# Optimization experiments

Measured on AMD Instinct MI355X. Metric: run time of the kernel, lower is better.

## Reference

```python
import jax, jax.numpy as jnp
import numpy as np
from jax import lax

TAU = 2.0      # LIF membrane time constant
VTH = 0.5      # spike threshold
ALPHA = 4.0    # sigmoid surrogate gradient sharpness (spikingjelly default)
EPS = 1e-5     # BatchNorm eps
HEADS = 8

@jax.custom_vjp
def _spike(x):
    return (x >= 0.0).astype(x.dtype)

def _spike_fwd(x):
    return _spike(x), x

def _spike_bwd(x, g):
    s = jax.nn.sigmoid(ALPHA * x)
    return (g * ALPHA * s * (1.0 - s),)

_spike.defvjp(_spike_fwd, _spike_bwd)

def lif(x_seq):
    # multi-step LIF, decay_input=True, hard reset to 0, detach_reset=True
    def step(v, x):
        v = v + (x - v) / TAU
        s = _spike(v - VTH)
        v = v * (1.0 - lax.stop_gradient(s))
        return v, s
    _, s_seq = lax.scan(step, jnp.zeros_like(x_seq[0]), x_seq)
    return s_seq

def bn(x, gamma, beta, mean, var):
    # inference-mode BatchNorm over channel axis 2 of [T,B,C,H,W]
    sh = (1, 1, -1, 1, 1)
    scale = gamma.reshape(sh) / jnp.sqrt(var.reshape(sh) + EPS)
    return (x - mean.reshape(sh)) * scale + beta.reshape(sh)

def conv1x1(x, w, b=None):
    y = jnp.einsum('oc,tbchw->tbohw', w, x)
    if b is not None:
        y = y + b.reshape(1, 1, -1, 1, 1)
    return y

def setup_inputs() -> dict:
    key = jax.random.key(0)
    T, B, C, H, W = 4, 8, 384, 32, 32
    ks = jax.random.split(key, 20)
    s = 1.0 / np.sqrt(C)
    d = {
        'x': jax.random.normal(ks[0], (T, B, C, H, W), jnp.float32),
        'q_w': jax.random.normal(ks[1], (C, C), jnp.float32) * s,
        'k_w': jax.random.normal(ks[2], (C, C), jnp.float32) * s,
        'v_w': jax.random.normal(ks[3], (C, C), jnp.float32) * s,
        'th_w': jax.random.normal(ks[4], (HEADS, HEADS), jnp.float32) * (1.0 / np.sqrt(HEADS)),
        'proj_w': jax.random.normal(ks[5], (C, C), jnp.float32) * s,
        'proj_b': jax.random.normal(ks[6], (C,), jnp.float32) * 0.01,
    }
    for i, p in enumerate(['q', 'k', 'v', 'proj']):
        kk = jax.random.split(ks[7 + i], 4)
        d[f'{p}_gamma'] = 1.0 + 0.1 * jax.random.normal(kk[0], (C,), jnp.float32)
        d[f'{p}_beta'] = 0.1 * jax.random.normal(kk[1], (C,), jnp.float32)
        d[f'{p}_mean'] = 0.1 * jax.random.normal(kk[2], (C,), jnp.float32)
        d[f'{p}_var'] = jax.random.uniform(kk[3], (C,), jnp.float32, 0.5, 1.5)
    return d

def reference(x, q_w, k_w, v_w, th_w, proj_w, proj_b,
              q_gamma, q_beta, q_mean, q_var,
              k_gamma, k_beta, k_mean, k_var,
              v_gamma, v_beta, v_mean, v_var,
              proj_gamma, proj_beta, proj_mean, proj_var):
    T, B, C, H, W = x.shape
    hd = C // HEADS
    N = H * W
    identity = x
    xs = lif(x)  # shortcut_lif

    def branch(w, g, be, m, va):
        return lif(bn(conv1x1(xs, w), g, be, m, va))

    def split_heads(t):  # [T,B,C,H,W] -> [T,B,heads,N,hd]
        return t.reshape(T, B, HEADS, hd, N).transpose(0, 1, 2, 4, 3)

    q = split_heads(branch(q_w, q_gamma, q_beta, q_mean, q_var))
    k = split_heads(branch(k_w, k_gamma, k_beta, k_mean, k_var))
    v = split_heads(branch(v_w, v_gamma, v_beta, v_mean, v_var))

    kv = (k * v).sum(axis=3)                      # [T,B,heads,hd]
    kv = jnp.einsum('oh,tbhd->tbod', th_w, kv)     # talking heads (Conv1d 1x1, no bias)
    kv = lif(kv)[:, :, :, None, :]                 # [T,B,heads,1,hd]

    x_att = q * kv                                 # broadcast over N
    x_att = x_att.transpose(0, 1, 2, 4, 3).reshape(T, B, C, H, W)
    out = bn(conv1x1(x_att, proj_w, proj_b), proj_gamma, proj_beta, proj_mean, proj_var)
    return out + identity
```

## Files before the change

### kernel.cpp

```cpp
#include <hip/hip_runtime.h>
#include <stdint.h>


typedef unsigned short u16;
typedef __attribute__((ext_vector_type(8))) short short8v;
typedef __attribute__((ext_vector_type(4))) float f32x4;

#define AS1 __attribute__((address_space(1)))
#define AS3 __attribute__((address_space(3)))

__device__ __forceinline__ void async16(const void* g, void* l) {
    __builtin_amdgcn_global_load_lds((const AS1 unsigned int*)g,
                                     (AS3 unsigned int*)l, 16, 0, 0);
}
__device__ __forceinline__ f32x4 mfma_bf16(short8v a, short8v b, f32x4 c) {
    return __builtin_amdgcn_mfma_f32_16x16x32_bf16(a, b, c, 0, 0, 0);
}
__device__ __forceinline__ f32x4 mfma_f16(short8v a, short8v b, f32x4 c) {
    return __builtin_amdgcn_mfma_f32_16x16x32_f16(a, b, c, 0, 0, 0);
}

__device__ __forceinline__ u16 f2bf(float f) {
    uint32_t x = __float_as_uint(f);
    return (u16)((x + 0x7FFFu + ((x >> 16) & 1u)) >> 16);
}

#define SPIKE_H ((u16)0x3C00)
#define SPIKE_B ((u16)0x3F80)

__global__ void prep_kernel(const float* __restrict__ qw, const float* __restrict__ kw,
                            const float* __restrict__ vw, const float* __restrict__ pw,
                            u16* __restrict__ Ah, u16* __restrict__ Aproj) {
    int id = blockIdx.x * 256 + threadIdx.x;
    if (id >= 1152 * 384) return;
    int m = id / 384, c = id % 384;
    int br = m / 384, o = m % 384;
    const float* W = (br == 0) ? qw : (br == 1) ? kw : vw;
    float w = W[o * 384 + c];
    union H { _Float16 h; u16 u; } u0, u1;
    u0.h = (_Float16)w;
    float r1 = w - (float)u0.h;
    u1.h = (_Float16)r1;
    u16* row = Ah + (size_t)m * 768;
    row[c] = u0.u;
    row[384 + c] = u1.u;
    if (br == 0) Aproj[o * 384 + c] = f2bf(pw[o * 384 + c]);
}

__global__ __launch_bounds__(256) void lifx_kernel(const float* __restrict__ x,
                                                   u16* __restrict__ xs) {
    __shared__ u16 Tr[64 * 72];
    int b = blockIdx.z, c0 = blockIdx.y * 64, n0 = blockIdx.x * 64;
    int tid = threadIdx.x;
    int nj = (tid & 15) * 4;
    int ci = tid >> 4;
    float v[4][4];
#pragma unroll
    for (int p = 0; p < 4; p++)
#pragma unroll
        for (int e = 0; e < 4; e++) v[p][e] = 0.0f;

    for (int t = 0; t < 4; t++) {
#pragma unroll
        for (int p = 0; p < 4; p++) {
            const float* src = x + ((size_t)((t * 8 + b) * 384 + c0 + p * 16 + ci)) * 1024 + n0 + nj;
            float4 xv = *(const float4*)src;
            float xa[4] = {xv.x, xv.y, xv.z, xv.w};
#pragma unroll
            for (int e = 0; e < 4; e++) {
                float vv = v[p][e];
                vv = __fadd_rn(vv, __fmul_rn(__fsub_rn(xa[e], vv), 0.5f));
                bool sp = (vv >= 0.5f);
                v[p][e] = sp ? 0.0f : vv;
                Tr[(nj + e) * 72 + p * 16 + ci] = sp ? SPIKE_H : (u16)0;
            }
        }
        __syncthreads();
#pragma unroll
        for (int p = 0; p < 4; p++) {
            int nr = p * 16 + (tid >> 4);
            int c4 = (tid & 15) * 4;
            *(ushort4*)(xs + ((size_t)((t * 8 + b) * 1024 + n0 + nr)) * 384 + c0 + c4) =
                *(const ushort4*)&Tr[nr * 72 + c4];
        }
        __syncthreads();
    }
}

__global__ __launch_bounds__(256, 2) void qkv_kernel(
    const u16* __restrict__ Ah, const u16* __restrict__ xs,
    u16* __restrict__ qs, u16* __restrict__ ks, u16* __restrict__ vs,
    const float* __restrict__ qg, const float* __restrict__ qb, const float* __restrict__ qm, const float* __restrict__ qv,
    const float* __restrict__ kg, const float* __restrict__ kb, const float* __restrict__ km, const float* __restrict__ kvr,
    const float* __restrict__ vg, const float* __restrict__ vb, const float* __restrict__ vm, const float* __restrict__ vvr) {
    __shared__ __align__(16) u16 At[2][8192];
    __shared__ __align__(16) u16 Bt[2][8192];
    __shared__ __align__(16) float bnS[128];
    __shared__ __align__(16) float bnM[128];
    __shared__ __align__(16) float bnB[128];

    int b = blockIdx.z, mt = blockIdx.y, nt = blockIdx.x;
    int m0 = mt * 128, n0 = nt * 128;
    int branch = mt / 3, o0 = (mt % 3) * 128;
    int tid = threadIdx.x, wave = tid >> 6, lane = tid & 63;
    int l15 = lane & 15, quad = lane >> 4;
    int wm = (wave & 1) * 64, wn = (wave >> 1) * 64;

    const float* g_ = (branch == 0) ? qg : (branch == 1) ? kg : vg;
    const float* be_ = (branch == 0) ? qb : (branch == 1) ? kb : vb;
    const float* m_ = (branch == 0) ? qm : (branch == 1) ? km : vm;
    const float* v_ = (branch == 0) ? qv : (branch == 1) ? kvr : vvr;
    u16* dstp = (branch == 0) ? qs : (branch == 1) ? ks : vs;

    if (tid < 128) {
        int o = o0 + tid;
        bnS[tid] = g_[o] / sqrtf(v_[o] + 1e-5f);
        bnM[tid] = m_[o];
        bnB[tid] = be_[o];
    }

    auto stage = [&](int s) {
        int st = s / 12, kkb = s % 12;
        int buf = s & 1;
        int kk = kkb * 64;
        int ck = (kk >= 384) ? kk - 384 : kk;
        const u16* Bsrc = xs + ((size_t)((st * 8 + b) * 1024 + n0)) * 384;
#pragma unroll
        for (int ii = 0; ii < 4; ii++) {
            int l = ii * 256 + tid;
            int row = l >> 3;
            int cs = (l & 7) ^ (row & 7);
            async16(Ah + (size_t)(m0 + row) * 768 + kk + cs * 8, &At[buf][l * 8]);
            async16(Bsrc + (size_t)row * 384 + ck + cs * 8, &Bt[buf][l * 8]);
        }
    };

    float vmem[4][4][4];
#pragma unroll
    for (int i = 0; i < 4; i++)
#pragma unroll
        for (int j = 0; j < 4; j++)
#pragma unroll
            for (int e = 0; e < 4; e++) vmem[i][j][e] = 0.0f;

    stage(0);
    __syncthreads();

    for (int t = 0; t < 4; t++) {
        f32x4 acc[4][4];
#pragma unroll
        for (int i = 0; i < 4; i++)
#pragma unroll
            for (int j = 0; j < 4; j++) acc[i][j] = (f32x4){0.f, 0.f, 0.f, 0.f};

        for (int kkb = 0; kkb < 12; kkb++) {
            int s = t * 12 + kkb;
            int buf = s & 1;
            if (s + 1 < 48) stage(s + 1);
#pragma unroll
            for (int h = 0; h < 2; h++) {
                short8v af[4], bfr[4];
#pragma unroll
                for (int i = 0; i < 4; i++) {
                    int row = wm + i * 16 + l15;
                    int ch = (h * 4 + quad) ^ (row & 7);
                    af[i] = *(const short8v*)&At[buf][row * 64 + ch * 8];
                }
#pragma unroll
                for (int j = 0; j < 4; j++) {
                    int nr = wn + j * 16 + l15;
                    int ch = (h * 4 + quad) ^ (nr & 7);
                    bfr[j] = *(const short8v*)&Bt[buf][nr * 64 + ch * 8];
                }
#pragma unroll
                for (int i = 0; i < 4; i++)
#pragma unroll
                    for (int j = 0; j < 4; j++) acc[i][j] = mfma_f16(af[i], bfr[j], acc[i][j]);
            }
            __syncthreads();
        }

        size_t rb = (size_t)((t * 8 + b) * 1024 + n0);
#pragma unroll
        for (int i = 0; i < 4; i++) {
            int co = wm + i * 16 + quad * 4;
            float4 sc4 = *(const float4*)&bnS[co];
            float4 mn4 = *(const float4*)&bnM[co];
            float4 bt4 = *(const float4*)&bnB[co];
            float scA[4] = {sc4.x, sc4.y, sc4.z, sc4.w};
            float mnA[4] = {mn4.x, mn4.y, mn4.z, mn4.w};
            float btA[4] = {bt4.x, bt4.y, bt4.z, bt4.w};
#pragma unroll
            for (int j = 0; j < 4; j++) {
                int n = wn + j * 16 + l15;
                u16 sv[4];
#pragma unroll
                for (int e = 0; e < 4; e++) {
                    float a = acc[i][j][e];
                    a = __fadd_rn(__fmul_rn(__fsub_rn(a, mnA[e]), scA[e]), btA[e]);
                    float vv = vmem[i][j][e];
                    vv = __fadd_rn(vv, __fmul_rn(__fsub_rn(a, vv), 0.5f));
                    bool sp = (vv >= 0.5f);
                    vmem[i][j][e] = sp ? 0.0f : vv;
                    sv[e] = sp ? SPIKE_B : (u16)0;
                }
                ushort4 s4;
                s4.x = sv[0]; s4.y = sv[1]; s4.z = sv[2]; s4.w = sv[3];
                *(ushort4*)(dstp + (rb + n) * 384 + o0 + co) = s4;
            }
        }
    }
}

__global__ void kvred_kernel(const u16* __restrict__ ks, const u16* __restrict__ vs,
                             float* __restrict__ r) {
    __shared__ float red[384];
    int tb = blockIdx.y, nc = blockIdx.x;
    int tid = threadIdx.x;
    int rr = tid / 48, c8 = tid % 48;
    red[tid] = 0.0f;
    __syncthreads();

    float cnt[8];
#pragma unroll
    for (int e = 0; e < 8; e++) cnt[e] = 0.0f;

    size_t base = ((size_t)(tb * 1024 + nc * 64 + rr)) * 384 + c8 * 8;
#pragma unroll 2
    for (int it = 0; it < 8; it++) {
        size_t off = base + (size_t)it * 8 * 384;
        uint4 ka = *(const uint4*)(ks + off);
        uint4 va = *(const uint4*)(vs + off);
        uint32_t w0 = ka.x & va.x, w1 = ka.y & va.y, w2 = ka.z & va.z, w3 = ka.w & va.w;
        const uint32_t S = SPIKE_B;
        if ((w0 & 0xFFFFu) == S) cnt[0] += 1.0f;
        if ((w0 >> 16) == S)     cnt[1] += 1.0f;
        if ((w1 & 0xFFFFu) == S) cnt[2] += 1.0f;
        if ((w1 >> 16) == S)     cnt[3] += 1.0f;
        if ((w2 & 0xFFFFu) == S) cnt[4] += 1.0f;
        if ((w2 >> 16) == S)     cnt[5] += 1.0f;
        if ((w3 & 0xFFFFu) == S) cnt[6] += 1.0f;
        if ((w3 >> 16) == S)     cnt[7] += 1.0f;
    }
#pragma unroll
    for (int e = 0; e < 8; e++) atomicAdd(&red[c8 * 8 + e], cnt[e]);
    __syncthreads();
    atomicAdd(&r[tb * 384 + tid], red[tid]);
}

__global__ void talking_kernel(const float* __restrict__ r, const float* __restrict__ th,
                               u16* __restrict__ kvs) {
    int id = blockIdx.x * 256 + threadIdx.x;
    if (id >= 8 * 384) return;
    int b = id / 384, c = id % 384;
    int oh = c / 48, d = c % 48;
    float v = 0.0f;
    for (int t = 0; t < 4; t++) {
        const float* rr = r + (t * 8 + b) * 384 + d;
        float s = 0.0f;
#pragma unroll
        for (int h = 0; h < 8; h++) s = __fmaf_rn(th[oh * 8 + h], rr[h * 48], s);
        v = __fadd_rn(v, __fmul_rn(__fsub_rn(s, v), 0.5f));
        bool sp = (v >= 0.5f);
        v = sp ? 0.0f : v;
        kvs[(t * 8 + b) * 384 + c] = sp ? SPIKE_B : (u16)0;
    }
}

__global__ __launch_bounds__(256, 2) void proj_kernel(
    const u16* __restrict__ Aproj, const u16* __restrict__ qs, const u16* __restrict__ kvs,
    const float* __restrict__ xin,
    const float* __restrict__ pb, const float* __restrict__ pg, const float* __restrict__ pbe,
    const float* __restrict__ pm, const float* __restrict__ pv, float* __restrict__ out) {
    __shared__ __align__(16) u16 At[2][8192];
    __shared__ __align__(16) u16 Bt[2][8192];

    int tb = blockIdx.z, mt = blockIdx.y, nt = blockIdx.x;
    int m0 = mt * 128, n0 = nt * 128;
    int tid = threadIdx.x, wave = tid >> 6, lane = tid & 63;
    int l15 = lane & 15, quad = lane >> 4;
    int wm = (wave & 1) * 64, wn = (wave >> 1) * 64;

    const u16* Bsrc = qs + ((size_t)(tb * 1024 + n0)) * 384;
    const u16* mbase = kvs + tb * 384;

    auto stage = [&](int s) {
        int kk = s * 64;
        int buf = s & 1;
#pragma unroll
        for (int ii = 0; ii < 4; ii++) {
            int l = ii * 256 + tid;
            int row = l >> 3;
            int cs = (l & 7) ^ (row & 7);
            async16(Aproj + (size_t)(m0 + row) * 384 + kk + cs * 8, &At[buf][l * 8]);
            async16(Bsrc + (size_t)row * 384 + kk + cs * 8, &Bt[buf][l * 8]);
        }
    };

    f32x4 acc[4][4];
#pragma unroll
    for (int i = 0; i < 4; i++)
#pragma unroll
        for (int j = 0; j < 4; j++) acc[i][j] = (f32x4){0.f, 0.f, 0.f, 0.f};

    stage(0);
    __syncthreads();

    for (int kkb = 0; kkb < 6; kkb++) {
        int buf = kkb & 1;
        int kk = kkb * 64;
        if (kkb + 1 < 6) stage(kkb + 1);
#pragma unroll
        for (int h = 0; h < 2; h++) {
            int g = h * 4 + quad;
            short8v msk = *(const short8v*)(mbase + kk + g * 8);
            short8v af[4], bfr[4];
#pragma unroll
            for (int i = 0; i < 4; i++) {
                int row = wm + i * 16 + l15;
                int ch = g ^ (row & 7);
                af[i] = *(const short8v*)&At[buf][row * 64 + ch * 8];
            }
#pragma unroll
            for (int j = 0; j < 4; j++) {
                int nr = wn + j * 16 + l15;
                int ch = g ^ (nr & 7);
                bfr[j] = *(const short8v*)&Bt[buf][nr * 64 + ch * 8] & msk;
            }
#pragma unroll
            for (int i = 0; i < 4; i++)
#pragma unroll
                for (int j = 0; j < 4; j++) acc[i][j] = mfma_bf16(af[i], bfr[j], acc[i][j]);
        }
        __syncthreads();
    }

#pragma unroll
    for (int i = 0; i < 4; i++) {
#pragma unroll
        for (int e = 0; e < 4; e++) {
            int o = m0 + wm + i * 16 + quad * 4 + e;
            float scale = pg[o] / sqrtf(pv[o] + 1e-5f);
            float mean = pm[o], beta = pbe[o], bias = pb[o];
#pragma unroll
            for (int j = 0; j < 4; j++) {
                int n = n0 + wn + j * 16 + l15;
                size_t idx = ((size_t)tb * 384 + o) * 1024 + n;
                float y = __fadd_rn(acc[i][j][e], bias);
                y = __fadd_rn(__fmul_rn(__fsub_rn(y, mean), scale), beta);
                out[idx] = __fadd_rn(y, xin[idx]);
            }
        }
    }
}

extern "C" void kernel_launch(void* const* d_in, const int* in_sizes, int n_in,
                              void* d_out, int out_size, void* d_ws, size_t ws_size,
                              hipStream_t stream) {
    (void)in_sizes; (void)n_in; (void)out_size; (void)ws_size;
    const float* x  = (const float*)d_in[0];
    const float* qw = (const float*)d_in[1];
    const float* kw = (const float*)d_in[2];
    const float* vw = (const float*)d_in[3];
    const float* th = (const float*)d_in[4];
    const float* pw = (const float*)d_in[5];
    const float* pb = (const float*)d_in[6];
    const float* qg = (const float*)d_in[7],  *qbe = (const float*)d_in[8];
    const float* qm = (const float*)d_in[9],  *qv  = (const float*)d_in[10];
    const float* kg = (const float*)d_in[11], *kbe = (const float*)d_in[12];
    const float* km = (const float*)d_in[13], *kv_ = (const float*)d_in[14];
    const float* vg = (const float*)d_in[15], *vbe = (const float*)d_in[16];
    const float* vm = (const float*)d_in[17], *vv_ = (const float*)d_in[18];
    const float* pg = (const float*)d_in[19], *pbe = (const float*)d_in[20];
    const float* pm = (const float*)d_in[21], *pv  = (const float*)d_in[22];
    float* out = (float*)d_out;

    char* w = (char*)d_ws;
    const size_t SPIKES = (size_t)32 * 1024 * 384 * 2;
    u16* xs    = (u16*)(w);
    u16* qs    = (u16*)(w + SPIKES);
    u16* ks    = (u16*)(w + 2 * SPIKES);
    u16* vs    = (u16*)(w + 3 * SPIKES);
    u16* Ah    = (u16*)(w + 4 * SPIKES);
    u16* Aproj = (u16*)(w + 4 * SPIKES + 1769472);
    float* r   = (float*)(w + 4 * SPIKES + 1769472 + 294912);
    u16* kvs   = (u16*)(w + 4 * SPIKES + 1769472 + 294912 + 49152);

    hipMemsetAsync(r, 0, 32 * 384 * sizeof(float), stream);

    prep_kernel<<<1728, 256, 0, stream>>>(qw, kw, vw, pw, Ah, Aproj);
    lifx_kernel<<<dim3(16, 6, 8), 256, 0, stream>>>(x, xs);
    qkv_kernel<<<dim3(8, 9, 8), 256, 0, stream>>>(Ah, xs, qs, ks, vs,
                                                  qg, qbe, qm, qv,
                                                  kg, kbe, km, kv_,
                                                  vg, vbe, vm, vv_);
    kvred_kernel<<<dim3(16, 32), 384, 0, stream>>>(ks, vs, r);
    talking_kernel<<<12, 256, 0, stream>>>(r, th, kvs);
    proj_kernel<<<dim3(8, 3, 32), 256, 0, stream>>>(Aproj, qs, kvs, x, pb, pg, pbe, pm, pv, out);
}
```

Baseline: 299.1 us.

## Restructure QKV GEMM to batch all timesteps into one 512-thread tile

The QKV kernel now uses 512 threads and loads B tiles for all four timesteps at once, so each A fragment is reused across four timesteps. A single 24-step K loop replaces the per-timestep loop, and the LIF recurrence runs over timesteps in registers in the epilogue. The loop uses a two-stage async prefetch with explicit vmcnt/lgkmcnt waits and barriers, plus s_setprio around the MFMA block. BN parameters are read directly from global memory instead of shared memory. The cost is a larger accumulator set (4x8 tiles per wave), which raises register pressure at launch bounds of 512 threads and 4 blocks.

Result: slower. 943.1 us (+215.4%).

```diff
diff --git a/kernel.cpp b/kernel.cpp
--- a/kernel.cpp
+++ b/kernel.cpp
@@ -87,126 +87,129 @@
     }
 }
 
-__global__ __launch_bounds__(256, 2) void qkv_kernel(
+__global__ __launch_bounds__(512, 4) void qkv_kernel(
     const u16* __restrict__ Ah, const u16* __restrict__ xs,
     u16* __restrict__ qs, u16* __restrict__ ks, u16* __restrict__ vs,
     const float* __restrict__ qg, const float* __restrict__ qb, const float* __restrict__ qm, const float* __restrict__ qv,
     const float* __restrict__ kg, const float* __restrict__ kb, const float* __restrict__ km, const float* __restrict__ kvr,
     const float* __restrict__ vg, const float* __restrict__ vb, const float* __restrict__ vm, const float* __restrict__ vvr) {
-    __shared__ __align__(16) u16 At[2][8192];
-    __shared__ __align__(16) u16 Bt[2][8192];
-    __shared__ __align__(16) float bnS[128];
-    __shared__ __align__(16) float bnM[128];
-    __shared__ __align__(16) float bnB[128];
+    __shared__ __align__(16) u16 At[2][4096];
+    __shared__ __align__(16) u16 Bt[2][16384];
 
     int b = blockIdx.z, mt = blockIdx.y, nt = blockIdx.x;
     int m0 = mt * 128, n0 = nt * 128;
     int branch = mt / 3, o0 = (mt % 3) * 128;
     int tid = threadIdx.x, wave = tid >> 6, lane = tid & 63;
     int l15 = lane & 15, quad = lane >> 4;
-    int wm = (wave & 1) * 64, wn = (wave >> 1) * 64;
-
-    const float* g_ = (branch == 0) ? qg : (branch == 1) ? kg : vg;
+    int wm = (wave & 1) * 64;
+    int wc = wave >> 1;
+
+    int arow = tid >> 2;
+    const u16* asrc = Ah + (size_t)(m0 + arow) * 768 + ((tid & 3) ^ (arow & 3)) * 8;
+    const u16* bsrc[4];
+#pragma unroll
+    for (int ii = 0; ii < 4; ii++) {
+        int l = ii * 512 + tid;
+        int col = l >> 2;
+        int cs = (l & 3) ^ (col & 3);
+        int t = col >> 7, nl = col & 127;
+        bsrc[ii] = xs + ((size_t)((t * 8 + b) * 1024 + n0 + nl)) * 384 + cs * 8;
+    }
+
+    auto stage = [&](int s) {
+        int buf = s & 1;
+        int kk = s * 32;
+        int ck = (kk >= 384) ? (kk - 384) : kk;
+        async16(asrc + kk, &At[buf][tid * 8]);
+#pragma unroll
+        for (int ii = 0; ii < 4; ii++)
+            async16(bsrc[ii] + ck, &Bt[buf][(ii * 512 + tid) * 8]);
+    };
+
+    int aoff[4], boff[8];
+#pragma unroll
+    for (int i = 0; i < 4; i++) {
+        int row = wm + i * 16 + l15;
+        aoff[i] = row * 32 + (quad ^ (row & 3)) * 8;
+    }
+#pragma unroll
+    for (int j = 0; j < 8; j++) {
+        int col = (j >> 1) * 128 + wc * 32 + (j & 1) * 16 + l15;
+        boff[j] = col * 32 + (quad ^ (col & 3)) * 8;
+    }
+
+    f32x4 acc[4][8];
+#pragma unroll
+    for (int i = 0; i < 4; i++)
+#pragma unroll
+        for (int j = 0; j < 8; j++) acc[i][j] = (f32x4){0.f, 0.f, 0.f, 0.f};
+
+    stage(0);
+    stage(1);
+
+#pragma unroll 1
+    for (int s = 0; s < 24; ++s) {
+        int buf = s & 1;
+        if (s < 23) asm volatile("s_waitcnt vmcnt(5)\n\ts_barrier" ::: "memory");
+        else        asm volatile("s_waitcnt vmcnt(0)\n\ts_barrier" ::: "memory");
+
+        short8v af[4], bf[8];
+#pragma unroll
+        for (int i = 0; i < 4; i++) af[i] = *(const short8v*)&At[buf][aoff[i]];
+#pragma unroll
+        for (int j = 0; j < 8; j++) bf[j] = *(const short8v*)&Bt[buf][boff[j]];
+
+        asm volatile("s_waitcnt lgkmcnt(0)\n\ts_barrier" ::: "memory");
+        if (s + 2 < 24) stage(s + 2);
+
+        __builtin_amdgcn_s_setprio(1);
+#pragma unroll
+        for (int i = 0; i < 4; i++)
+#pragma unroll
+            for (int j = 0; j < 8; j++) acc[i][j] = mfma_f16(af[i], bf[j], acc[i][j]);
+        __builtin_amdgcn_s_setprio(0);
+    }
+
+    const float* g_  = (branch == 0) ? qg : (branch == 1) ? kg : vg;
     const float* be_ = (branch == 0) ? qb : (branch == 1) ? kb : vb;
-    const float* m_ = (branch == 0) ? qm : (branch == 1) ? km : vm;
-    const float* v_ = (branch == 0) ? qv : (branch == 1) ? kvr : vvr;
+    const float* m_  = (branch == 0) ? qm : (branch == 1) ? km : vm;
+    const float* v_  = (branch == 0) ? qv : (branch == 1) ? kvr : vvr;
     u16* dstp = (branch == 0) ? qs : (branch == 1) ? ks : vs;
 
-    if (tid < 128) {
-        int o = o0 + tid;
-        bnS[tid] = g_[o] / sqrtf(v_[o] + 1e-5f);
-        bnM[tid] = m_[o];
-        bnB[tid] = be_[o];
-    }
-
-    auto stage = [&](int s) {
-        int st = s / 12, kkb = s % 12;
-        int buf = s & 1;
-        int kk = kkb * 64;
-        int ck = (kk >= 384) ? kk - 384 : kk;
-        const u16* Bsrc = xs + ((size_t)((st * 8 + b) * 1024 + n0)) * 384;
-#pragma unroll
-        for (int ii = 0; ii < 4; ii++) {
-            int l = ii * 256 + tid;
-            int row = l >> 3;
-            int cs = (l & 7) ^ (row & 7);
-            async16(Ah + (size_t)(m0 + row) * 768 + kk + cs * 8, &At[buf][l * 8]);
-            async16(Bsrc + (size_t)row * 384 + ck + cs * 8, &Bt[buf][l * 8]);
-        }
-    };
-
-    float vmem[4][4][4];
-#pragma unroll
-    for (int i = 0; i < 4; i++)
-#pragma unroll
-        for (int j = 0; j < 4; j++)
-#pragma unroll
-            for (int e = 0; e < 4; e++) vmem[i][j][e] = 0.0f;
-
-    stage(0);
-    __syncthreads();
-
-    for (int t = 0; t < 4; t++) {
-        f32x4 acc[4][4];
-#pragma unroll
-        for (int i = 0; i < 4; i++)
-#pragma unroll
-            for (int j = 0; j < 4; j++) acc[i][j] = (f32x4){0.f, 0.f, 0.f, 0.f};
-
-        for (int kkb = 0; kkb < 12; kkb++) {
-            int s = t * 12 + kkb;
-            int buf = s & 1;
-            if (s + 1 < 48) stage(s + 1);
-#pragma unroll
-            for (int h = 0; h < 2; h++) {
-                short8v af[4], bfr[4];
-#pragma unroll
-                for (int i = 0; i < 4; i++) {
-                    int row = wm + i * 16 + l15;
-                    int ch = (h * 4 + quad) ^ (row & 7);
-                    af[i] = *(const short8v*)&At[buf][row * 64 + ch * 8];
-                }
-#pragma unroll
-                for (int j = 0; j < 4; j++) {
-                    int nr = wn + j * 16 + l15;
-                    int ch = (h * 4 + quad) ^ (nr & 7);
-                    bfr[j] = *(const short8v*)&Bt[buf][nr * 64 + ch * 8];
-                }
-#pragma unroll
-                for (int i = 0; i < 4; i++)
-#pragma unroll
-                    for (int j = 0; j < 4; j++) acc[i][j] = mfma_f16(af[i], bfr[j], acc[i][j]);
-            }
-            __syncthreads();
-        }
-
-        size_t rb = (size_t)((t * 8 + b) * 1024 + n0);
-#pragma unroll
-        for (int i = 0; i < 4; i++) {
-            int co = wm + i * 16 + quad * 4;
-            float4 sc4 = *(const float4*)&bnS[co];
-            float4 mn4 = *(const float4*)&bnM[co];
-            float4 bt4 = *(const float4*)&bnB[co];
-            float scA[4] = {sc4.x, sc4.y, sc4.z, sc4.w};
-            float mnA[4] = {mn4.x, mn4.y, mn4.z, mn4.w};
-            float btA[4] = {bt4.x, bt4.y, bt4.z, bt4.w};
-#pragma unroll
-            for (int j = 0; j < 4; j++) {
-                int n = wn + j * 16 + l15;
-                u16 sv[4];
-#pragma unroll
-                for (int e = 0; e < 4; e++) {
-                    float a = acc[i][j][e];
-                    a = __fadd_rn(__fmul_rn(__fsub_rn(a, mnA[e]), scA[e]), btA[e]);
-                    float vv = vmem[i][j][e];
+#pragma unroll
+    for (int i = 0; i < 4; i++) {
+        int co = wm + i * 16 + quad * 4;
+        int o = o0 + co;
+        float4 g4  = *(const float4*)&g_[o];
+        float4 va4 = *(const float4*)&v_[o];
+        float4 mn4 = *(const float4*)&m_[o];
+        float4 be4 = *(const float4*)&be_[o];
+        float sc[4] = {g4.x / sqrtf(va4.x + 1e-5f), g4.y / sqrtf(va4.y + 1e-5f),
+                       g4.z / sqrtf(va4.z + 1e-5f), g4.w / sqrtf(va4.w + 1e-5f)};
+        float mn[4] = {mn4.x, mn4.y, mn4.z, mn4.w};
+        float bt[4] = {be4.x, be4.y, be4.z, be4.w};
+#pragma unroll
+        for (int h = 0; h < 2; h++) {
+            int n = n0 + wc * 32 + h * 16 + l15;
+            u16 sv[4][4];
+#pragma unroll
+            for (int e = 0; e < 4; e++) {
+                float vv = 0.0f;
+#pragma unroll
+                for (int t = 0; t < 4; t++) {
+                    float a = acc[i][t * 2 + h][e];
+                    a = __fadd_rn(__fmul_rn(__fsub_rn(a, mn[e]), sc[e]), bt[e]);
                     vv = __fadd_rn(vv, __fmul_rn(__fsub_rn(a, vv), 0.5f));
                     bool sp = (vv >= 0.5f);
-                    vmem[i][j][e] = sp ? 0.0f : vv;
-                    sv[e] = sp ? SPIKE_B : (u16)0;
+                    vv = sp ? 0.0f : vv;
+                    sv[t][e] = sp ? SPIKE_B : (u16)0;
                 }
+            }
+#pragma unroll
+            for (int t = 0; t < 4; t++) {
                 ushort4 s4;
-                s4.x = sv[0]; s4.y = sv[1]; s4.z = sv[2]; s4.w = sv[3];
-                *(ushort4*)(dstp + (rb + n) * 384 + o0 + co) = s4;
+                s4.x = sv[t][0]; s4.y = sv[t][1]; s4.z = sv[t][2]; s4.w = sv[t][3];
+                *(ushort4*)(dstp + ((size_t)((t * 8 + b) * 1024 + n)) * 384 + o) = s4;
             }
         }
     }
@@ -390,7 +393,7 @@
 
     prep_kernel<<<1728, 256, 0, stream>>>(qw, kw, vw, pw, Ah, Aproj);
     lifx_kernel<<<dim3(16, 6, 8), 256, 0, stream>>>(x, xs);
-    qkv_kernel<<<dim3(8, 9, 8), 256, 0, stream>>>(Ah, xs, qs, ks, vs,
+    qkv_kernel<<<dim3(8, 9, 8), 512, 0, stream>>>(Ah, xs, qs, ks, vs,
                                                   qg, qbe, qm, qv,
                                                   kg, kbe, km, kv_,
                                                   vg, vbe, vm, vv_);
```
